# Optimization experiments

Hardware: AMD Instinct MI355X
Metric: run time of the kernel (lower is better)

## Reference

```python
import jax, jax.numpy as jnp
import numpy as np

N_NODES = 100000
N_EDGES = 300000
N_BOUNDARY = 1024
N_VERTS = 4        # n_verts[i]; selects out_layers[3] = Linear(fc_n, 12)
CONVS = [3, 64, 128, 256]
FC_N = 256


def _uniform(k, shape, fan_in):
    s = 1.0 / np.sqrt(fan_in)
    return jax.random.uniform(k, shape, minval=-s, maxval=s, dtype=jnp.float32)


def setup_inputs() -> dict:
    key = jax.random.key(0)
    ks = jax.random.split(key, 32)
    inp = {}
    inp['vs'] = jax.random.normal(ks[0], (N_NODES, 3), dtype=jnp.float32)
    inp['edges'] = jax.random.randint(ks[1], (N_EDGES, 2), 0, N_NODES)
    inp['boundary_idx'] = jax.random.randint(ks[2], (N_BOUNDARY,), 0, N_NODES)
    inp['n_verts'] = N_VERTS
    ki = 3
    for j in range(len(CONVS) - 1):
        cin, cout = CONVS[j], CONVS[j + 1]
        inp[f'W_self{j}'] = _uniform(ks[ki], (cin, cout), cin); ki += 1
        inp[f'W_nbr{j}'] = _uniform(ks[ki], (cin, cout), cin); ki += 1
        inp[f'b{j}'] = _uniform(ks[ki], (cout,), cin); ki += 1
    inp['W_dense'] = _uniform(ks[ki], (CONVS[-1], FC_N), CONVS[-1]); ki += 1
    inp['b_dense'] = _uniform(ks[ki], (FC_N,), CONVS[-1]); ki += 1
    inp['W_out'] = _uniform(ks[ki], (FC_N, 3 * N_VERTS), FC_N); ki += 1
    inp['b_out'] = _uniform(ks[ki], (3 * N_VERTS,), FC_N)
    return inp


def graph_conv(x, edges, W_self, W_nbr, b):
    # out_i = x_i @ W_self + (sum_{j in N(i)} x_j) @ W_nbr + b, symmetric edges
    n = x.shape[0]
    src, dst = edges[:, 0], edges[:, 1]
    agg = jax.ops.segment_sum(x[src], dst, num_segments=n)
    agg = agg + jax.ops.segment_sum(x[dst], src, num_segments=n)
    return x @ W_self + agg @ W_nbr + b


def reference(vs, edges, boundary_idx, n_verts,
              W_self0, W_nbr0, b0, W_self1, W_nbr1, b1, W_self2, W_nbr2, b2,
              W_dense, b_dense, W_out, b_out):
    boundary_mean = jnp.mean(vs[boundary_idx], axis=0)  # (3,)
    x = vs
    for Ws, Wn, b in ((W_self0, W_nbr0, b0), (W_self1, W_nbr1, b1), (W_self2, W_nbr2, b2)):
        x = jax.nn.relu(graph_conv(x, edges, Ws, Wn, b))
    pooled = jnp.mean(x[boundary_idx], axis=0, keepdims=True)  # (1, C)
    h = jax.nn.relu(pooled @ W_dense + b_dense)                # (1, FC_N)
    out = (h @ W_out + b_out).reshape((n_verts, 3))
    return boundary_mean + out
```

## Files before the change

kernel.cpp:

```cpp
#include <hip/hip_runtime.h>

#define N_NODES 100000
#define N_EDGES 300000
#define NB 1024

#define CAP_F1 16384
#define CAP_F2 65536
#define K_ADJ  64

#define CNT_F1 0
#define CNT_F2 16

#define OFF_X1C     0u
#define OFF_X2C     4194304u
#define OFF_X3B     6291456u
#define OFF_AGG0C   6553600u
#define OFF_AGG1C   6815744u
#define OFF_AGG2C   7864320u
#define OFF_POOL    7995392u
#define OFF_CNT     7995648u
#define OFF_DEGF2   7995712u
#define OFF_DEGF1   8061248u
#define OFF_DEGB    8077632u
#define OFF_MF1     8078656u
#define OFF_MF2     8178656u
#define ZERO_END    8278656u
#define ZERO_BYTES  ((ZERO_END - OFF_POOL) * 4u)
#define OFF_SLOTB   8278656u
#define FF_BYTES    (100000u * 4u)
#define OFF_SLOTF1  8378656u
#define OFF_SLOTF2  8478656u
#define OFF_LISTF1  8578656u
#define OFF_LISTF2  8595040u
#define OFF_ADJ0    8660576u
#define OFF_ADJF1   12854880u
#define OFF_ADJB    13903456u
#define OFF_IDXX2   13968992u
#define OFF_IDXA2   13970016u
#define OFF_F1F2    13971040u
#define OFF_BMEAN   13987424u

__global__ void bmean_kernel(const float* __restrict__ vs, const int* __restrict__ bidx,
                             float* __restrict__ bmean) {
    int tid = threadIdx.x;
    float s0 = 0.f, s1 = 0.f, s2 = 0.f;
    for (int i = tid; i < NB; i += 256) {
        int n = bidx[i];
        s0 += vs[n * 3 + 0];
        s1 += vs[n * 3 + 1];
        s2 += vs[n * 3 + 2];
    }
    for (int off = 32; off > 0; off >>= 1) {
        s0 += __shfl_down(s0, off);
        s1 += __shfl_down(s1, off);
        s2 += __shfl_down(s2, off);
    }
    __shared__ float red[4][3];
    int wave = tid >> 6;
    if ((tid & 63) == 0) { red[wave][0] = s0; red[wave][1] = s1; red[wave][2] = s2; }
    __syncthreads();
    if (tid == 0) {
        float t0 = 0, t1 = 0, t2 = 0;
        for (int w = 0; w < 4; w++) { t0 += red[w][0]; t1 += red[w][1]; t2 += red[w][2]; }
        bmean[0] = t0 / NB; bmean[1] = t1 / NB; bmean[2] = t2 / NB;
    }
}

__global__ void mark_b_kernel(const int* __restrict__ bidx, int* __restrict__ slotB) {
    int i = blockIdx.x * 256 + threadIdx.x;
    if (i < NB) slotB[bidx[i]] = i;
}

__global__ void scan_mark_kernel(const int2* __restrict__ edges, const int* __restrict__ srcSlot,
                                 int* __restrict__ mark) {
    int e = blockIdx.x * 256 + threadIdx.x;
    if (e >= N_EDGES) return;
    int2 ed = edges[e];
    if (srcSlot[ed.y] >= 0) mark[ed.x] = 1;
    if (srcSlot[ed.x] >= 0) mark[ed.y] = 1;
}

__global__ __launch_bounds__(256) void compact_kernel(
        const int* __restrict__ mark, const int* __restrict__ aux,
        int* __restrict__ slot, int* __restrict__ list,
        int* __restrict__ cnt, int cap, int* __restrict__ f1map) {
    int i = blockIdx.x * 256 + threadIdx.x;
    int auxv = -1;
    bool want = false;
    if (i < N_NODES) {
        auxv = aux[i];
        want = (mark[i] != 0) || (auxv >= 0);
    }
    int wave = threadIdx.x >> 6, lane = threadIdx.x & 63;
    unsigned long long m = __ballot(want);
    int rank = __popcll(m & ((1ull << lane) - 1));
    __shared__ int s_w[4];
    __shared__ int s_base;
    if (lane == 0) s_w[wave] = __popcll(m);
    __syncthreads();
    if (threadIdx.x == 0) {
        int s = 0;
        #pragma unroll
        for (int w = 0; w < 4; w++) { int v = s_w[w]; s_w[w] = s; s += v; }
        s_base = s ? atomicAdd(cnt, s) : 0;
    }
    __syncthreads();
    if (i < N_NODES) {
        int p = -1;
        if (want) {
            p = s_base + s_w[wave] + rank;
            if (p < cap) list[p] = i; else p = -1;
        }
        slot[i] = p;
        if (f1map && auxv >= 0) f1map[auxv] = p;
    }
}

__device__ __forceinline__ void adj_append(int* __restrict__ deg, int* __restrict__ adj,
                                           int slot, int src) {
    int pos = atomicAdd(&deg[slot], 1);
    if (pos < K_ADJ) adj[slot * K_ADJ + pos] = src;
}

__global__ void build_adj_kernel(const int2* __restrict__ edges,
                                 const int* __restrict__ slotB, const int* __restrict__ slotF1,
                                 const int* __restrict__ slotF2,
                                 int* __restrict__ degF2, int* __restrict__ adj0,
                                 int* __restrict__ degF1, int* __restrict__ adjF1,
                                 int* __restrict__ degB, int* __restrict__ adjB) {
    int e = blockIdx.x * 256 + threadIdx.x;
    if (e >= N_EDGES) return;
    int2 ed = edges[e];
    int x = ed.x, y = ed.y;
    int sxB = slotB[x], syB = slotB[y];
    int sxF1 = slotF1[x], syF1 = slotF1[y];
    int sxF2 = slotF2[x], syF2 = slotF2[y];
    if (syF2 >= 0) adj_append(degF2, adj0, syF2, x);
    if (sxF2 >= 0) adj_append(degF2, adj0, sxF2, y);
    if (syF1 >= 0) adj_append(degF1, adjF1, syF1, sxF2);
    if (sxF1 >= 0) adj_append(degF1, adjF1, sxF1, syF2);
    if (syB >= 0)  adj_append(degB, adjB, syB, sxF1);
    if (sxB >= 0)  adj_append(degB, adjB, sxB, syF1);
}

__global__ void conv2_idx_kernel(const int* __restrict__ bidx, const int* __restrict__ slotB,
                                 const int* __restrict__ slotF1,
                                 int* __restrict__ idxx, int* __restrict__ idxa) {
    int i = blockIdx.x * 256 + threadIdx.x;
    if (i >= NB) return;
    int n = bidx[i];
    idxx[i] = slotF1[n];
    idxa[i] = slotB[n];
}

__global__ void gather0_kernel(const float* __restrict__ vs, const int* __restrict__ adj0,
                               const int* __restrict__ degF2, const int* __restrict__ cnt,
                               float* __restrict__ agg0c) {
    int s = blockIdx.x * 256 + threadIdx.x;
    int n = min(cnt[CNT_F2], CAP_F2);
    if (s >= n) return;
    int deg = min(degF2[s], K_ADJ);
    float a0 = 0.f, a1 = 0.f, a2 = 0.f;
    for (int d = 0; d < deg; d++) {
        int src = adj0[s * K_ADJ + d];
        a0 += vs[src * 3 + 0];
        a1 += vs[src * 3 + 1];
        a2 += vs[src * 3 + 2];
    }
    agg0c[s * 4 + 0] = a0; agg0c[s * 4 + 1] = a1; agg0c[s * 4 + 2] = a2;
}

__global__ void conv0c_kernel(const float* __restrict__ vs, const int* __restrict__ listF2,
                              const float* __restrict__ agg0c,
                              const float* __restrict__ Ws, const float* __restrict__ Wn,
                              const float* __restrict__ b, const int* __restrict__ cnt,
                              float* __restrict__ x1c) {
    int nF2 = min(cnt[CNT_F2], CAP_F2);
    if ((int)blockIdx.x * 4 >= nF2) return;
    __shared__ float ws_l[192], wn_l[192], b_l[64];
    int tid = threadIdx.x;
    if (tid < 192) { ws_l[tid] = Ws[tid]; wn_l[tid] = Wn[tid]; }
    if (tid < 64) b_l[tid] = b[tid];
    __syncthreads();
    int g = blockIdx.x * 4 + (tid >> 6);
    int j = tid & 63;
    if (g >= nF2) return;
    int n = listF2[g];
    float x0 = vs[n * 3 + 0], x1v = vs[n * 3 + 1], x2v = vs[n * 3 + 2];
    float a0 = agg0c[g * 4 + 0], a1 = agg0c[g * 4 + 1], a2 = agg0c[g * 4 + 2];
    float acc = b_l[j];
    acc = fmaf(x0, ws_l[0 * 64 + j], acc);
    acc = fmaf(x1v, ws_l[1 * 64 + j], acc);
    acc = fmaf(x2v, ws_l[2 * 64 + j], acc);
    acc = fmaf(a0, wn_l[0 * 64 + j], acc);
    acc = fmaf(a1, wn_l[1 * 64 + j], acc);
    acc = fmaf(a2, wn_l[2 * 64 + j], acc);
    x1c[g * 64 + j] = fmaxf(acc, 0.f);
}

__global__ __launch_bounds__(256) void gather1_kernel(const float* __restrict__ x1c,
                                                      const int* __restrict__ adjF1,
                                                      const int* __restrict__ degF1,
                                                      const int* __restrict__ cnt,
                                                      float* __restrict__ agg1c) {
    int wslot = blockIdx.x * 4 + (threadIdx.x >> 6);
    int lane = threadIdx.x & 63;
    int n = min(cnt[CNT_F1], CAP_F1);
    if (wslot >= n) return;
    int deg = min(degF1[wslot], K_ADJ);
    float acc = 0.f;
    for (int d = 0; d < deg; d++) {
        int src = adjF1[wslot * K_ADJ + d];
        if (src >= 0) acc += x1c[src * 64 + lane];
    }
    agg1c[wslot * 64 + lane] = acc;
}

__global__ __launch_bounds__(256) void gather2_kernel(const float* __restrict__ x2c,
                                                      const int* __restrict__ adjB,
                                                      const int* __restrict__ degB,
                                                      float* __restrict__ agg2c) {
    int wslot = blockIdx.x * 4 + (threadIdx.x >> 6);
    int lane = threadIdx.x & 63;
    int deg = min(degB[wslot], K_ADJ);
    float a0 = 0.f, a1 = 0.f;
    for (int d = 0; d < deg; d++) {
        int src = adjB[wslot * K_ADJ + d];
        if (src >= 0) {
            a0 += x2c[src * 128 + lane];
            a1 += x2c[src * 128 + 64 + lane];
        }
    }
    agg2c[wslot * 128 + lane] = a0;
    agg2c[wslot * 128 + 64 + lane] = a1;
}

template <int CIN, int COUT, int ROWS>
__global__ __launch_bounds__(256) void convT_kernel(
    const float* __restrict__ x, const float* __restrict__ agg,
    const float* __restrict__ Ws, const float* __restrict__ Wn,
    const float* __restrict__ b, float* __restrict__ out,
    const int* __restrict__ idxx, const int* __restrict__ idxa,
    int nrows_max, const int* __restrict__ nrows_dev) {
    const int RPT = ROWS / 4;
    const int C4 = CIN / 4;
    const int UNR = 16;
    __shared__ float xs[ROWS * CIN];
    __shared__ float as[ROWS * CIN];
    int nrows = nrows_max;
    if (nrows_dev) { int nd = nrows_dev[0]; nrows = nd < nrows ? nd : nrows; }
    int gbase = blockIdx.x * ROWS;
    if (gbase >= nrows) return;
    int tid = threadIdx.x;
    int cb = blockIdx.y * 64;
    for (int i = tid; i < ROWS * C4; i += 256) {
        int nl = i / C4, c4 = i % C4;
        int ng = gbase + nl;
        float4 xv = make_float4(0.f, 0.f, 0.f, 0.f);
        float4 av = xv;
        if (ng < nrows) {
            int rowx = idxx ? idxx[ng] : ng;
            int rowa = idxa ? idxa[ng] : ng;
            xv = ((const float4*)x)[rowx * C4 + c4];
            av = ((const float4*)agg)[rowa * C4 + c4];
        }
        ((float4*)xs)[i] = xv;
        ((float4*)as)[i] = av;
    }
    __syncthreads();
    int j = tid & 63, g = tid >> 6;
    const float* Wsp = Ws + cb + j;
    const float* Wnp = Wn + cb + j;
    float acc[RPT];
    float bv = b[cb + j];
    #pragma unroll
    for (int k = 0; k < RPT; k++) acc[k] = bv;
    float w0[2 * UNR];
    #pragma unroll
    for (int u = 0; u < UNR; u++) {
        w0[u]       = Wsp[u * COUT];
        w0[UNR + u] = Wnp[u * COUT];
    }
    for (int cc = 0; cc < CIN; cc += UNR) {
        float w1[2 * UNR];
        bool more = (cc + UNR) < CIN;
        if (more) {
            #pragma unroll
            for (int u = 0; u < UNR; u++) {
                w1[u]       = Wsp[(cc + UNR + u) * COUT];
                w1[UNR + u] = Wnp[(cc + UNR + u) * COUT];
            }
        }
        #pragma unroll
        for (int u = 0; u < UNR; u++) {
            float wsv = w0[u], wnv = w0[UNR + u];
            #pragma unroll
            for (int k = 0; k < RPT; k++) {
                float xv = xs[(g * RPT + k) * CIN + cc + u];
                float av = as[(g * RPT + k) * CIN + cc + u];
                acc[k] = fmaf(xv, wsv, fmaf(av, wnv, acc[k]));
            }
        }
        if (more) {
            #pragma unroll
            for (int u = 0; u < 2 * UNR; u++) w0[u] = w1[u];
        }
    }
    #pragma unroll
    for (int k = 0; k < RPT; k++) {
        int ng = gbase + g * RPT + k;
        if (ng < nrows) out[ng * COUT + cb + j] = fmaxf(acc[k], 0.f);
    }
}

__global__ void pool_kernel(const float* __restrict__ x3b, float* __restrict__ pooled) {
    int j = threadIdx.x;
    int r0 = blockIdx.x * 32;
    float s = 0.f;
    for (int r = 0; r < 32; r++) s += x3b[(r0 + r) * 256 + j];
    atomicAdd(&pooled[j], s);
}

__global__ void head_kernel(const float* __restrict__ pooled_sum, const float* __restrict__ bmean,
                            const float* __restrict__ Wd, const float* __restrict__ bd,
                            const float* __restrict__ Wo, const float* __restrict__ bo,
                            float* __restrict__ out) {
    __shared__ float p_l[256], h_l[256];
    int tid = threadIdx.x;
    p_l[tid] = pooled_sum[tid] * (1.0f / NB);
    __syncthreads();
    float acc = bd[tid];
    for (int c = 0; c < 256; c++) acc = fmaf(p_l[c], Wd[c * 256 + tid], acc);
    h_l[tid] = fmaxf(acc, 0.f);
    __syncthreads();
    if (tid < 12) {
        float o = bo[tid];
        for (int c = 0; c < 256; c++) o = fmaf(h_l[c], Wo[c * 12 + tid], o);
        out[tid] = o + bmean[tid % 3];
    }
}

extern "C" void kernel_launch(void* const* d_in, const int* in_sizes, int n_in,
                              void* d_out, int out_size, void* d_ws, size_t ws_size,
                              hipStream_t stream) {
    const float* vs    = (const float*)d_in[0];
    const int2*  edges = (const int2*)d_in[1];
    const int*   bidx  = (const int*)d_in[2];
    const float* Ws0 = (const float*)d_in[4];
    const float* Wn0 = (const float*)d_in[5];
    const float* b0  = (const float*)d_in[6];
    const float* Ws1 = (const float*)d_in[7];
    const float* Wn1 = (const float*)d_in[8];
    const float* b1  = (const float*)d_in[9];
    const float* Ws2 = (const float*)d_in[10];
    const float* Wn2 = (const float*)d_in[11];
    const float* b2  = (const float*)d_in[12];
    const float* Wd  = (const float*)d_in[13];
    const float* bd  = (const float*)d_in[14];
    const float* Wo  = (const float*)d_in[15];
    const float* bo  = (const float*)d_in[16];

    float* ws = (float*)d_ws;
    float* x1c    = ws + OFF_X1C;
    float* x2c    = ws + OFF_X2C;
    float* x3b    = ws + OFF_X3B;
    float* agg0c  = ws + OFF_AGG0C;
    float* agg1c  = ws + OFF_AGG1C;
    float* agg2c  = ws + OFF_AGG2C;
    float* pooled = ws + OFF_POOL;
    int*   cnt    = (int*)(ws + OFF_CNT);
    int*   degF2  = (int*)(ws + OFF_DEGF2);
    int*   degF1  = (int*)(ws + OFF_DEGF1);
    int*   degB   = (int*)(ws + OFF_DEGB);
    int*   mF1    = (int*)(ws + OFF_MF1);
    int*   mF2    = (int*)(ws + OFF_MF2);
    int*   slotB  = (int*)(ws + OFF_SLOTB);
    int*   slotF1 = (int*)(ws + OFF_SLOTF1);
    int*   slotF2 = (int*)(ws + OFF_SLOTF2);
    int*   listF1 = (int*)(ws + OFF_LISTF1);
    int*   listF2 = (int*)(ws + OFF_LISTF2);
    int*   adj0   = (int*)(ws + OFF_ADJ0);
    int*   adjF1  = (int*)(ws + OFF_ADJF1);
    int*   adjB   = (int*)(ws + OFF_ADJB);
    int*   idxx2  = (int*)(ws + OFF_IDXX2);
    int*   idxa2  = (int*)(ws + OFF_IDXA2);
    int*   f1f2   = (int*)(ws + OFF_F1F2);
    float* bmean  = ws + OFF_BMEAN;
    float* outp   = (float*)d_out;

    const int EB = (N_EDGES + 255) / 256;
    const int NBLK = (N_NODES + 255) / 256;

    hipMemsetAsync(ws + OFF_POOL, 0, ZERO_BYTES, stream);
    hipMemsetAsync(ws + OFF_SLOTB, 0xFF, FF_BYTES, stream);

    bmean_kernel<<<1, 256, 0, stream>>>(vs, bidx, bmean);

    mark_b_kernel<<<(NB + 255) / 256, 256, 0, stream>>>(bidx, slotB);
    scan_mark_kernel<<<EB, 256, 0, stream>>>(edges, slotB, mF1);
    compact_kernel<<<NBLK, 256, 0, stream>>>(mF1, slotB, slotF1, listF1,
                                             cnt + CNT_F1, CAP_F1, nullptr);
    scan_mark_kernel<<<EB, 256, 0, stream>>>(edges, slotF1, mF2);
    compact_kernel<<<NBLK, 256, 0, stream>>>(mF2, slotF1, slotF2, listF2,
                                             cnt + CNT_F2, CAP_F2, f1f2);
    build_adj_kernel<<<EB, 256, 0, stream>>>(edges, slotB, slotF1, slotF2,
                                             degF2, adj0, degF1, adjF1, degB, adjB);
    conv2_idx_kernel<<<(NB + 255) / 256, 256, 0, stream>>>(bidx, slotB, slotF1, idxx2, idxa2);

    gather0_kernel<<<CAP_F2 / 256, 256, 0, stream>>>(vs, adj0, degF2, cnt, agg0c);
    conv0c_kernel<<<CAP_F2 / 4, 256, 0, stream>>>(vs, listF2, agg0c, Ws0, Wn0, b0, cnt, x1c);

    gather1_kernel<<<CAP_F1 / 4, 256, 0, stream>>>(x1c, adjF1, degF1, cnt, agg1c);
    convT_kernel<64, 128, 16><<<dim3(CAP_F1 / 16, 2), 256, 0, stream>>>(
        x1c, agg1c, Ws1, Wn1, b1, x2c, f1f2, nullptr, CAP_F1, cnt + CNT_F1);

    gather2_kernel<<<NB / 4, 256, 0, stream>>>(x2c, adjB, degB, agg2c);
    convT_kernel<128, 256, 8><<<dim3(NB / 8, 4), 256, 0, stream>>>(
        x2c, agg2c, Ws2, Wn2, b2, x3b, idxx2, idxa2, NB, nullptr);

    pool_kernel<<<32, 256, 0, stream>>>(x3b, pooled);
    head_kernel<<<1, 256, 0, stream>>>(pooled, bmean, Wd, bd, Wo, bo, outp);
}
```

Baseline: 232.9 us.

## Fuse frontier-building stages into one cooperative kernel and fuse gather/pool into convs

Replaces the chain of small preprocessing kernels (boundary mean, marking, two compactions, adjacency build, index setup) with a single cooperative kernel that separates phases with grid-wide syncs. The layer-0 neighbor gather is folded into the conv0 kernel using one wave per node and a shuffle reduction, and pooling is folded into the last conv through shared and global atomics. This cuts launch overhead and intermediate buffers, but grid.sync costs and the fixed 1024-block cooperative grid may limit parallelism. The pooled sum's floating-point order now depends on atomic timing.

```diff
diff --git a/kernel.cpp b/kernel.cpp
--- a/kernel.cpp
+++ b/kernel.cpp
@@ -1,4 +1,7 @@
 #include <hip/hip_runtime.h>
+#include <hip/hip_cooperative_groups.h>
+
+namespace cg = cooperative_groups;
 
 #define N_NODES 100000
 #define N_EDGES 300000
@@ -11,10 +14,11 @@
 #define CNT_F1 0
 #define CNT_F2 16
 
+#define FGRID  1024
+
 #define OFF_X1C     0u
 #define OFF_X2C     4194304u
 #define OFF_X3B     6291456u
-#define OFF_AGG0C   6553600u
 #define OFF_AGG1C   6815744u
 #define OFF_AGG2C   7864320u
 #define OFF_POOL    7995392u
@@ -38,143 +42,143 @@
 #define OFF_IDXX2   13968992u
 #define OFF_IDXA2   13970016u
 #define OFF_F1F2    13971040u
-#define OFF_BMEAN   13987424u
-
-__global__ void bmean_kernel(const float* __restrict__ vs, const int* __restrict__ bidx,
-                             float* __restrict__ bmean) {
-    int tid = threadIdx.x;
-    float s0 = 0.f, s1 = 0.f, s2 = 0.f;
-    for (int i = tid; i < NB; i += 256) {
-        int n = bidx[i];
-        s0 += vs[n * 3 + 0];
-        s1 += vs[n * 3 + 1];
-        s2 += vs[n * 3 + 2];
-    }
-    for (int off = 32; off > 0; off >>= 1) {
-        s0 += __shfl_down(s0, off);
-        s1 += __shfl_down(s1, off);
-        s2 += __shfl_down(s2, off);
-    }
-    __shared__ float red[4][3];
-    int wave = tid >> 6;
-    if ((tid & 63) == 0) { red[wave][0] = s0; red[wave][1] = s1; red[wave][2] = s2; }
-    __syncthreads();
-    if (tid == 0) {
-        float t0 = 0, t1 = 0, t2 = 0;
-        for (int w = 0; w < 4; w++) { t0 += red[w][0]; t1 += red[w][1]; t2 += red[w][2]; }
-        bmean[0] = t0 / NB; bmean[1] = t1 / NB; bmean[2] = t2 / NB;
-    }
-}
-
-__global__ void mark_b_kernel(const int* __restrict__ bidx, int* __restrict__ slotB) {
-    int i = blockIdx.x * 256 + threadIdx.x;
-    if (i < NB) slotB[bidx[i]] = i;
-}
-
-__global__ void scan_mark_kernel(const int2* __restrict__ edges, const int* __restrict__ srcSlot,
-                                 int* __restrict__ mark) {
-    int e = blockIdx.x * 256 + threadIdx.x;
-    if (e >= N_EDGES) return;
-    int2 ed = edges[e];
-    if (srcSlot[ed.y] >= 0) mark[ed.x] = 1;
-    if (srcSlot[ed.x] >= 0) mark[ed.y] = 1;
-}
-
-__global__ __launch_bounds__(256) void compact_kernel(
+#define OFF_BSUM    13987424u
+#define OFF_BMEAN   13990496u
+
+struct FArgs {
+    const float* vs; const int2* edges; const int* bidx;
+    int* slotB; int* mF1; int* slotF1; int* listF1;
+    int* mF2; int* slotF2; int* listF2; int* f1f2;
+    int* cnt; int* degF2; int* adj0; int* degF1; int* adjF1;
+    int* degB; int* adjB; int* idxx; int* idxa;
+    float* bsum; float* bmean;
+};
+
+__device__ __forceinline__ void adj_append(int* __restrict__ deg, int* __restrict__ adj,
+                                           int slot, int src) {
+    int pos = atomicAdd(&deg[slot], 1);
+    if (pos < K_ADJ) adj[slot * K_ADJ + pos] = src;
+}
+
+__device__ __forceinline__ void compact_phase(
+        int i, int lane, int wave, int tidx,
         const int* __restrict__ mark, const int* __restrict__ aux,
         int* __restrict__ slot, int* __restrict__ list,
-        int* __restrict__ cnt, int cap, int* __restrict__ f1map) {
-    int i = blockIdx.x * 256 + threadIdx.x;
+        int* __restrict__ cnt, int cap, int* __restrict__ f1map,
+        int* s_w, int* s_base) {
     int auxv = -1;
     bool want = false;
     if (i < N_NODES) {
         auxv = aux[i];
         want = (mark[i] != 0) || (auxv >= 0);
     }
-    int wave = threadIdx.x >> 6, lane = threadIdx.x & 63;
     unsigned long long m = __ballot(want);
     int rank = __popcll(m & ((1ull << lane) - 1));
-    __shared__ int s_w[4];
-    __shared__ int s_base;
     if (lane == 0) s_w[wave] = __popcll(m);
     __syncthreads();
-    if (threadIdx.x == 0) {
+    if (tidx == 0) {
         int s = 0;
         #pragma unroll
         for (int w = 0; w < 4; w++) { int v = s_w[w]; s_w[w] = s; s += v; }
-        s_base = s ? atomicAdd(cnt, s) : 0;
+        s_base[0] = s ? atomicAdd(cnt, s) : 0;
     }
     __syncthreads();
     if (i < N_NODES) {
         int p = -1;
         if (want) {
-            p = s_base + s_w[wave] + rank;
+            p = s_base[0] + s_w[wave] + rank;
             if (p < cap) list[p] = i; else p = -1;
         }
         slot[i] = p;
         if (f1map && auxv >= 0) f1map[auxv] = p;
     }
-}
-
-__device__ __forceinline__ void adj_append(int* __restrict__ deg, int* __restrict__ adj,
-                                           int slot, int src) {
-    int pos = atomicAdd(&deg[slot], 1);
-    if (pos < K_ADJ) adj[slot * K_ADJ + pos] = src;
-}
-
-__global__ void build_adj_kernel(const int2* __restrict__ edges,
-                                 const int* __restrict__ slotB, const int* __restrict__ slotF1,
-                                 const int* __restrict__ slotF2,
-                                 int* __restrict__ degF2, int* __restrict__ adj0,
-                                 int* __restrict__ degF1, int* __restrict__ adjF1,
-                                 int* __restrict__ degB, int* __restrict__ adjB) {
-    int e = blockIdx.x * 256 + threadIdx.x;
-    if (e >= N_EDGES) return;
-    int2 ed = edges[e];
-    int x = ed.x, y = ed.y;
-    int sxB = slotB[x], syB = slotB[y];
-    int sxF1 = slotF1[x], syF1 = slotF1[y];
-    int sxF2 = slotF2[x], syF2 = slotF2[y];
-    if (syF2 >= 0) adj_append(degF2, adj0, syF2, x);
-    if (sxF2 >= 0) adj_append(degF2, adj0, sxF2, y);
-    if (syF1 >= 0) adj_append(degF1, adjF1, syF1, sxF2);
-    if (sxF1 >= 0) adj_append(degF1, adjF1, sxF1, syF2);
-    if (syB >= 0)  adj_append(degB, adjB, syB, sxF1);
-    if (sxB >= 0)  adj_append(degB, adjB, sxB, syF1);
-}
-
-__global__ void conv2_idx_kernel(const int* __restrict__ bidx, const int* __restrict__ slotB,
-                                 const int* __restrict__ slotF1,
-                                 int* __restrict__ idxx, int* __restrict__ idxa) {
-    int i = blockIdx.x * 256 + threadIdx.x;
-    if (i >= NB) return;
-    int n = bidx[i];
-    idxx[i] = slotF1[n];
-    idxa[i] = slotB[n];
-}
-
-__global__ void gather0_kernel(const float* __restrict__ vs, const int* __restrict__ adj0,
-                               const int* __restrict__ degF2, const int* __restrict__ cnt,
-                               float* __restrict__ agg0c) {
-    int s = blockIdx.x * 256 + threadIdx.x;
-    int n = min(cnt[CNT_F2], CAP_F2);
-    if (s >= n) return;
-    int deg = min(degF2[s], K_ADJ);
-    float a0 = 0.f, a1 = 0.f, a2 = 0.f;
-    for (int d = 0; d < deg; d++) {
-        int src = adj0[s * K_ADJ + d];
-        a0 += vs[src * 3 + 0];
-        a1 += vs[src * 3 + 1];
-        a2 += vs[src * 3 + 2];
-    }
-    agg0c[s * 4 + 0] = a0; agg0c[s * 4 + 1] = a1; agg0c[s * 4 + 2] = a2;
-}
-
-__global__ void conv0c_kernel(const float* __restrict__ vs, const int* __restrict__ listF2,
-                              const float* __restrict__ agg0c,
-                              const float* __restrict__ Ws, const float* __restrict__ Wn,
-                              const float* __restrict__ b, const int* __restrict__ cnt,
-                              float* __restrict__ x1c) {
+    __syncthreads();
+}
+
+__global__ void __launch_bounds__(256) frontier_kernel(FArgs a) {
+    cg::grid_group grid = cg::this_grid();
+    const int tid0 = blockIdx.x * 256 + threadIdx.x;
+    const int stride = gridDim.x * 256;
+    const int lane = threadIdx.x & 63, wave = threadIdx.x >> 6;
+    __shared__ int s_w[4];
+    __shared__ int s_base[1];
+    __shared__ float s_red[4][3];
+
+    float s0 = 0.f, s1 = 0.f, s2 = 0.f;
+    for (int i = tid0; i < NB; i += stride) {
+        int n = a.bidx[i];
+        a.slotB[n] = i;
+        s0 += a.vs[n * 3 + 0]; s1 += a.vs[n * 3 + 1]; s2 += a.vs[n * 3 + 2];
+    }
+    for (int off = 32; off > 0; off >>= 1) {
+        s0 += __shfl_down(s0, off); s1 += __shfl_down(s1, off); s2 += __shfl_down(s2, off);
+    }
+    if (lane == 0) { s_red[wave][0] = s0; s_red[wave][1] = s1; s_red[wave][2] = s2; }
+    __syncthreads();
+    if (threadIdx.x == 0) {
+        float t0 = 0, t1 = 0, t2 = 0;
+        for (int w = 0; w < 4; w++) { t0 += s_red[w][0]; t1 += s_red[w][1]; t2 += s_red[w][2]; }
+        a.bsum[blockIdx.x * 3 + 0] = t0;
+        a.bsum[blockIdx.x * 3 + 1] = t1;
+        a.bsum[blockIdx.x * 3 + 2] = t2;
+    }
+    grid.sync();
+
+    for (int e = tid0; e < N_EDGES; e += stride) {
+        int2 ed = a.edges[e];
+        if (a.slotB[ed.y] >= 0) a.mF1[ed.x] = 1;
+        if (a.slotB[ed.x] >= 0) a.mF1[ed.y] = 1;
+    }
+    if (blockIdx.x == 0 && threadIdx.x < 192) {
+        int c = threadIdx.x >> 6, l = threadIdx.x & 63;
+        float p = 0.f;
+        for (int k = l; k < (int)gridDim.x; k += 64) p += a.bsum[k * 3 + c];
+        for (int off = 32; off > 0; off >>= 1) p += __shfl_down(p, off);
+        if (l == 0) a.bmean[c] = p / NB;
+    }
+    grid.sync();
+
+    compact_phase(tid0, lane, wave, threadIdx.x, a.mF1, a.slotB,
+                  a.slotF1, a.listF1, a.cnt + CNT_F1, CAP_F1, nullptr, s_w, s_base);
+    grid.sync();
+
+    for (int e = tid0; e < N_EDGES; e += stride) {
+        int2 ed = a.edges[e];
+        if (a.slotF1[ed.y] >= 0) a.mF2[ed.x] = 1;
+        if (a.slotF1[ed.x] >= 0) a.mF2[ed.y] = 1;
+    }
+    grid.sync();
+
+    compact_phase(tid0, lane, wave, threadIdx.x, a.mF2, a.slotF1,
+                  a.slotF2, a.listF2, a.cnt + CNT_F2, CAP_F2, a.f1f2, s_w, s_base);
+    grid.sync();
+
+    for (int e = tid0; e < N_EDGES; e += stride) {
+        int2 ed = a.edges[e];
+        int x = ed.x, y = ed.y;
+        int sxB = a.slotB[x], syB = a.slotB[y];
+        int sxF1 = a.slotF1[x], syF1 = a.slotF1[y];
+        int sxF2 = a.slotF2[x], syF2 = a.slotF2[y];
+        if (syF2 >= 0) adj_append(a.degF2, a.adj0, syF2, x);
+        if (sxF2 >= 0) adj_append(a.degF2, a.adj0, sxF2, y);
+        if (syF1 >= 0) adj_append(a.degF1, a.adjF1, syF1, sxF2);
+        if (sxF1 >= 0) adj_append(a.degF1, a.adjF1, sxF1, syF2);
+        if (syB >= 0)  adj_append(a.degB, a.adjB, syB, sxF1);
+        if (sxB >= 0)  adj_append(a.degB, a.adjB, sxB, syF1);
+    }
+    for (int i = tid0; i < NB; i += stride) {
+        int n = a.bidx[i];
+        a.idxx[i] = a.slotF1[n];
+        a.idxa[i] = a.slotB[n];
+    }
+}
+
+__global__ __launch_bounds__(256) void conv0f_kernel(
+        const float* __restrict__ vs, const int* __restrict__ listF2,
+        const int* __restrict__ adj0, const int* __restrict__ degF2,
+        const float* __restrict__ Ws, const float* __restrict__ Wn,
+        const float* __restrict__ b, const int* __restrict__ cnt,
+        float* __restrict__ x1c) {
     int nF2 = min(cnt[CNT_F2], CAP_F2);
     if ((int)blockIdx.x * 4 >= nF2) return;
     __shared__ float ws_l[192], wn_l[192], b_l[64];
@@ -182,20 +186,29 @@
     if (tid < 192) { ws_l[tid] = Ws[tid]; wn_l[tid] = Wn[tid]; }
     if (tid < 64) b_l[tid] = b[tid];
     __syncthreads();
-    int g = blockIdx.x * 4 + (tid >> 6);
-    int j = tid & 63;
-    if (g >= nF2) return;
-    int n = listF2[g];
+    int s = blockIdx.x * 4 + (tid >> 6);
+    int lane = tid & 63;
+    if (s >= nF2) return;
+    int deg = min(degF2[s], K_ADJ);
+    float a0 = 0.f, a1 = 0.f, a2 = 0.f;
+    if (lane < deg) {
+        int src = adj0[s * K_ADJ + lane];
+        a0 = vs[src * 3 + 0]; a1 = vs[src * 3 + 1]; a2 = vs[src * 3 + 2];
+    }
+    for (int off = 32; off > 0; off >>= 1) {
+        a0 += __shfl_down(a0, off); a1 += __shfl_down(a1, off); a2 += __shfl_down(a2, off);
+    }
+    a0 = __shfl(a0, 0); a1 = __shfl(a1, 0); a2 = __shfl(a2, 0);
+    int n = listF2[s];
     float x0 = vs[n * 3 + 0], x1v = vs[n * 3 + 1], x2v = vs[n * 3 + 2];
-    float a0 = agg0c[g * 4 + 0], a1 = agg0c[g * 4 + 1], a2 = agg0c[g * 4 + 2];
-    float acc = b_l[j];
-    acc = fmaf(x0, ws_l[0 * 64 + j], acc);
-    acc = fmaf(x1v, ws_l[1 * 64 + j], acc);
-    acc = fmaf(x2v, ws_l[2 * 64 + j], acc);
-    acc = fmaf(a0, wn_l[0 * 64 + j], acc);
-    acc = fmaf(a1, wn_l[1 * 64 + j], acc);
-    acc = fmaf(a2, wn_l[2 * 64 + j], acc);
-    x1c[g * 64 + j] = fmaxf(acc, 0.f);
+    float acc = b_l[lane];
+    acc = fmaf(x0, ws_l[0 * 64 + lane], acc);
+    acc = fmaf(x1v, ws_l[1 * 64 + lane], acc);
+    acc = fmaf(x2v, ws_l[2 * 64 + lane], acc);
+    acc = fmaf(a0, wn_l[0 * 64 + lane], acc);
+    acc = fmaf(a1, wn_l[1 * 64 + lane], acc);
+    acc = fmaf(a2, wn_l[2 * 64 + lane], acc);
+    x1c[s * 64 + lane] = fmaxf(acc, 0.f);
 }
 
 __global__ __launch_bounds__(256) void gather1_kernel(const float* __restrict__ x1c,
@@ -235,7 +248,7 @@
     agg2c[wslot * 128 + 64 + lane] = a1;
 }
 
-template <int CIN, int COUT, int ROWS>
+template <int CIN, int COUT, int ROWS, bool POOL>
 __global__ __launch_bounds__(256) void convT_kernel(
     const float* __restrict__ x, const float* __restrict__ agg,
     const float* __restrict__ Ws, const float* __restrict__ Wn,
@@ -247,12 +260,14 @@
     const int UNR = 16;
     __shared__ float xs[ROWS * CIN];
     __shared__ float as[ROWS * CIN];
+    __shared__ float psum[64];
     int nrows = nrows_max;
     if (nrows_dev) { int nd = nrows_dev[0]; nrows = nd < nrows ? nd : nrows; }
     int gbase = blockIdx.x * ROWS;
     if (gbase >= nrows) return;
     int tid = threadIdx.x;
     int cb = blockIdx.y * 64;
+    if (POOL && tid < 64) psum[tid] = 0.f;
     for (int i = tid; i < ROWS * C4; i += 256) {
         int nl = i / C4, c4 = i % C4;
         int ng = gbase + nl;
@@ -306,19 +321,23 @@
             for (int u = 0; u < 2 * UNR; u++) w0[u] = w1[u];
         }
     }
-    #pragma unroll
-    for (int k = 0; k < RPT; k++) {
-        int ng = gbase + g * RPT + k;
-        if (ng < nrows) out[ng * COUT + cb + j] = fmaxf(acc[k], 0.f);
-    }
-}
-
-__global__ void pool_kernel(const float* __restrict__ x3b, float* __restrict__ pooled) {
-    int j = threadIdx.x;
-    int r0 = blockIdx.x * 32;
-    float s = 0.f;
-    for (int r = 0; r < 32; r++) s += x3b[(r0 + r) * 256 + j];
-    atomicAdd(&pooled[j], s);
+    if (POOL) {
+        float part = 0.f;
+        #pragma unroll
+        for (int k = 0; k < RPT; k++) {
+            int ng = gbase + g * RPT + k;
+            if (ng < nrows) part += fmaxf(acc[k], 0.f);
+        }
+        atomicAdd(&psum[j], part);
+        __syncthreads();
+        if (tid < 64) atomicAdd(&out[cb + tid], psum[tid]);
+    } else {
+        #pragma unroll
+        for (int k = 0; k < RPT; k++) {
+            int ng = gbase + g * RPT + k;
+            if (ng < nrows) out[ng * COUT + cb + j] = fmaxf(acc[k], 0.f);
+        }
+    }
 }
 
 __global__ void head_kernel(const float* __restrict__ pooled_sum, const float* __restrict__ bmean,
@@ -363,61 +382,52 @@
     float* ws = (float*)d_ws;
     float* x1c    = ws + OFF_X1C;
     float* x2c    = ws + OFF_X2C;
-    float* x3b    = ws + OFF_X3B;
-    float* agg0c  = ws + OFF_AGG0C;
     float* agg1c  = ws + OFF_AGG1C;
     float* agg2c  = ws + OFF_AGG2C;
     float* pooled = ws + OFF_POOL;
     int*   cnt    = (int*)(ws + OFF_CNT);
-    int*   degF2  = (int*)(ws + OFF_DEGF2);
-    int*   degF1  = (int*)(ws + OFF_DEGF1);
-    int*   degB   = (int*)(ws + OFF_DEGB);
-    int*   mF1    = (int*)(ws + OFF_MF1);
-    int*   mF2    = (int*)(ws + OFF_MF2);
-    int*   slotB  = (int*)(ws + OFF_SLOTB);
-    int*   slotF1 = (int*)(ws + OFF_SLOTF1);
-    int*   slotF2 = (int*)(ws + OFF_SLOTF2);
-    int*   listF1 = (int*)(ws + OFF_LISTF1);
-    int*   listF2 = (int*)(ws + OFF_LISTF2);
-    int*   adj0   = (int*)(ws + OFF_ADJ0);
-    int*   adjF1  = (int*)(ws + OFF_ADJF1);
-    int*   adjB   = (int*)(ws + OFF_ADJB);
-    int*   idxx2  = (int*)(ws + OFF_IDXX2);
-    int*   idxa2  = (int*)(ws + OFF_IDXA2);
-    int*   f1f2   = (int*)(ws + OFF_F1F2);
     float* bmean  = ws + OFF_BMEAN;
     float* outp   = (float*)d_out;
 
-    const int EB = (N_EDGES + 255) / 256;
-    const int NBLK = (N_NODES + 255) / 256;
+    FArgs fa;
+    fa.vs = vs; fa.edges = edges; fa.bidx = bidx;
+    fa.slotB  = (int*)(ws + OFF_SLOTB);
+    fa.mF1    = (int*)(ws + OFF_MF1);
+    fa.slotF1 = (int*)(ws + OFF_SLOTF1);
+    fa.listF1 = (int*)(ws + OFF_LISTF1);
+    fa.mF2    = (int*)(ws + OFF_MF2);
+    fa.slotF2 = (int*)(ws + OFF_SLOTF2);
+    fa.listF2 = (int*)(ws + OFF_LISTF2);
+    fa.f1f2   = (int*)(ws + OFF_F1F2);
+    fa.cnt    = cnt;
+    fa.degF2  = (int*)(ws + OFF_DEGF2);
+    fa.adj0   = (int*)(ws + OFF_ADJ0);
+    fa.degF1  = (int*)(ws + OFF_DEGF1);
+    fa.adjF1  = (int*)(ws + OFF_ADJF1);
+    fa.degB   = (int*)(ws + OFF_DEGB);
+    fa.adjB   = (int*)(ws + OFF_ADJB);
+    fa.idxx   = (int*)(ws + OFF_IDXX2);
+    fa.idxa   = (int*)(ws + OFF_IDXA2);
+    fa.bsum   = ws + OFF_BSUM;
+    fa.bmean  = bmean;
 
     hipMemsetAsync(ws + OFF_POOL, 0, ZERO_BYTES, stream);
     hipMemsetAsync(ws + OFF_SLOTB, 0xFF, FF_BYTES, stream);
 
-    bmean_kernel<<<1, 256, 0, stream>>>(vs, bidx, bmean);
-
-    mark_b_kernel<<<(NB + 255) / 256, 256, 0, stream>>>(bidx, slotB);
-    scan_mark_kernel<<<EB, 256, 0, stream>>>(edges, slotB, mF1);
-    compact_kernel<<<NBLK, 256, 0, stream>>>(mF1, slotB, slotF1, listF1,
-                                             cnt + CNT_F1, CAP_F1, nullptr);
-    scan_mark_kernel<<<EB, 256, 0, stream>>>(edges, slotF1, mF2);
-    compact_kernel<<<NBLK, 256, 0, stream>>>(mF2, slotF1, slotF2, listF2,
-                                             cnt + CNT_F2, CAP_F2, f1f2);
-    build_adj_kernel<<<EB, 256, 0, stream>>>(edges, slotB, slotF1, slotF2,
-                                             degF2, adj0, degF1, adjF1, degB, adjB);
-    conv2_idx_kernel<<<(NB + 255) / 256, 256, 0, stream>>>(bidx, slotB, slotF1, idxx2, idxa2);
-
-    gather0_kernel<<<CAP_F2 / 256, 256, 0, stream>>>(vs, adj0, degF2, cnt, agg0c);
-    conv0c_kernel<<<CAP_F2 / 4, 256, 0, stream>>>(vs, listF2, agg0c, Ws0, Wn0, b0, cnt, x1c);
-
-    gather1_kernel<<<CAP_F1 / 4, 256, 0, stream>>>(x1c, adjF1, degF1, cnt, agg1c);
-    convT_kernel<64, 128, 16><<<dim3(CAP_F1 / 16, 2), 256, 0, stream>>>(
-        x1c, agg1c, Ws1, Wn1, b1, x2c, f1f2, nullptr, CAP_F1, cnt + CNT_F1);
-
-    gather2_kernel<<<NB / 4, 256, 0, stream>>>(x2c, adjB, degB, agg2c);
-    convT_kernel<128, 256, 8><<<dim3(NB / 8, 4), 256, 0, stream>>>(
-        x2c, agg2c, Ws2, Wn2, b2, x3b, idxx2, idxa2, NB, nullptr);
-
-    pool_kernel<<<32, 256, 0, stream>>>(x3b, pooled);
+    void* kargs[] = { (void*)&fa };
+    hipLaunchCooperativeKernel((const void*)frontier_kernel,
+                               dim3(FGRID), dim3(256), kargs, 0, stream);
+
+    conv0f_kernel<<<CAP_F2 / 4, 256, 0, stream>>>(
+        vs, fa.listF2, fa.adj0, fa.degF2, Ws0, Wn0, b0, cnt, x1c);
+
+    gather1_kernel<<<CAP_F1 / 4, 256, 0, stream>>>(x1c, fa.adjF1, fa.degF1, cnt, agg1c);
+    convT_kernel<64, 128, 16, false><<<dim3(CAP_F1 / 16, 2), 256, 0, stream>>>(
+        x1c, agg1c, Ws1, Wn1, b1, x2c, fa.f1f2, nullptr, CAP_F1, cnt + CNT_F1);
+
+    gather2_kernel<<<NB / 4, 256, 0, stream>>>(x2c, fa.adjB, fa.degB, agg2c);
+    convT_kernel<128, 256, 8, true><<<dim3(NB / 8, 4), 256, 0, stream>>>(
+        x2c, agg2c, Ws2, Wn2, b2, pooled, fa.idxx, fa.idxa, NB, nullptr);
+
     head_kernel<<<1, 256, 0, stream>>>(pooled, bmean, Wd, bd, Wo, bo, outp);
 }
```

New measurement: 808.2 us. 247% more time.

## Fuse layer-0 gather into conv and pooling into final conv epilogue

Applied to the files above, without the earlier changes.

Merges the layer-0 neighbour gather into the conv0 kernel, using one wavefront per node with lane-parallel neighbour loads and a shuffle reduction. Folds the mean-pool into the last graph-conv kernel via shared-memory atomics followed by global atomics. This drops two kernel launches and the agg0/x3 intermediate buffers. In exchange it adds atomic contention on the pooled vector and summation order that varies between runs.

```diff
diff --git a/kernel.cpp b/kernel.cpp
--- a/kernel.cpp
+++ b/kernel.cpp
@@ -13,8 +13,6 @@
 
 #define OFF_X1C     0u
 #define OFF_X2C     4194304u
-#define OFF_X3B     6291456u
-#define OFF_AGG0C   6553600u
 #define OFF_AGG1C   6815744u
 #define OFF_AGG2C   7864320u
 #define OFF_POOL    7995392u
@@ -153,28 +151,12 @@
     idxa[i] = slotB[n];
 }
 
-__global__ void gather0_kernel(const float* __restrict__ vs, const int* __restrict__ adj0,
-                               const int* __restrict__ degF2, const int* __restrict__ cnt,
-                               float* __restrict__ agg0c) {
-    int s = blockIdx.x * 256 + threadIdx.x;
-    int n = min(cnt[CNT_F2], CAP_F2);
-    if (s >= n) return;
-    int deg = min(degF2[s], K_ADJ);
-    float a0 = 0.f, a1 = 0.f, a2 = 0.f;
-    for (int d = 0; d < deg; d++) {
-        int src = adj0[s * K_ADJ + d];
-        a0 += vs[src * 3 + 0];
-        a1 += vs[src * 3 + 1];
-        a2 += vs[src * 3 + 2];
-    }
-    agg0c[s * 4 + 0] = a0; agg0c[s * 4 + 1] = a1; agg0c[s * 4 + 2] = a2;
-}
-
-__global__ void conv0c_kernel(const float* __restrict__ vs, const int* __restrict__ listF2,
-                              const float* __restrict__ agg0c,
-                              const float* __restrict__ Ws, const float* __restrict__ Wn,
-                              const float* __restrict__ b, const int* __restrict__ cnt,
-                              float* __restrict__ x1c) {
+__global__ __launch_bounds__(256) void conv0f_kernel(
+        const float* __restrict__ vs, const int* __restrict__ listF2,
+        const int* __restrict__ adj0, const int* __restrict__ degF2,
+        const float* __restrict__ Ws, const float* __restrict__ Wn,
+        const float* __restrict__ b, const int* __restrict__ cnt,
+        float* __restrict__ x1c) {
     int nF2 = min(cnt[CNT_F2], CAP_F2);
     if ((int)blockIdx.x * 4 >= nF2) return;
     __shared__ float ws_l[192], wn_l[192], b_l[64];
@@ -182,20 +164,29 @@
     if (tid < 192) { ws_l[tid] = Ws[tid]; wn_l[tid] = Wn[tid]; }
     if (tid < 64) b_l[tid] = b[tid];
     __syncthreads();
-    int g = blockIdx.x * 4 + (tid >> 6);
-    int j = tid & 63;
-    if (g >= nF2) return;
-    int n = listF2[g];
+    int s = blockIdx.x * 4 + (tid >> 6);
+    int lane = tid & 63;
+    if (s >= nF2) return;
+    int deg = min(degF2[s], K_ADJ);
+    float a0 = 0.f, a1 = 0.f, a2 = 0.f;
+    if (lane < deg) {
+        int src = adj0[s * K_ADJ + lane];
+        a0 = vs[src * 3 + 0]; a1 = vs[src * 3 + 1]; a2 = vs[src * 3 + 2];
+    }
+    for (int off = 32; off > 0; off >>= 1) {
+        a0 += __shfl_down(a0, off); a1 += __shfl_down(a1, off); a2 += __shfl_down(a2, off);
+    }
+    a0 = __shfl(a0, 0); a1 = __shfl(a1, 0); a2 = __shfl(a2, 0);
+    int n = listF2[s];
     float x0 = vs[n * 3 + 0], x1v = vs[n * 3 + 1], x2v = vs[n * 3 + 2];
-    float a0 = agg0c[g * 4 + 0], a1 = agg0c[g * 4 + 1], a2 = agg0c[g * 4 + 2];
-    float acc = b_l[j];
-    acc = fmaf(x0, ws_l[0 * 64 + j], acc);
-    acc = fmaf(x1v, ws_l[1 * 64 + j], acc);
-    acc = fmaf(x2v, ws_l[2 * 64 + j], acc);
-    acc = fmaf(a0, wn_l[0 * 64 + j], acc);
-    acc = fmaf(a1, wn_l[1 * 64 + j], acc);
-    acc = fmaf(a2, wn_l[2 * 64 + j], acc);
-    x1c[g * 64 + j] = fmaxf(acc, 0.f);
+    float acc = b_l[lane];
+    acc = fmaf(x0, ws_l[0 * 64 + lane], acc);
+    acc = fmaf(x1v, ws_l[1 * 64 + lane], acc);
+    acc = fmaf(x2v, ws_l[2 * 64 + lane], acc);
+    acc = fmaf(a0, wn_l[0 * 64 + lane], acc);
+    acc = fmaf(a1, wn_l[1 * 64 + lane], acc);
+    acc = fmaf(a2, wn_l[2 * 64 + lane], acc);
+    x1c[s * 64 + lane] = fmaxf(acc, 0.f);
 }
 
 __global__ __launch_bounds__(256) void gather1_kernel(const float* __restrict__ x1c,
@@ -235,7 +226,7 @@
     agg2c[wslot * 128 + 64 + lane] = a1;
 }
 
-template <int CIN, int COUT, int ROWS>
+template <int CIN, int COUT, int ROWS, bool POOL>
 __global__ __launch_bounds__(256) void convT_kernel(
     const float* __restrict__ x, const float* __restrict__ agg,
     const float* __restrict__ Ws, const float* __restrict__ Wn,
@@ -247,12 +238,14 @@
     const int UNR = 16;
     __shared__ float xs[ROWS * CIN];
     __shared__ float as[ROWS * CIN];
+    __shared__ float psum[64];
     int nrows = nrows_max;
     if (nrows_dev) { int nd = nrows_dev[0]; nrows = nd < nrows ? nd : nrows; }
     int gbase = blockIdx.x * ROWS;
     if (gbase >= nrows) return;
     int tid = threadIdx.x;
     int cb = blockIdx.y * 64;
+    if (POOL && tid < 64) psum[tid] = 0.f;
     for (int i = tid; i < ROWS * C4; i += 256) {
         int nl = i / C4, c4 = i % C4;
         int ng = gbase + nl;
@@ -306,19 +299,23 @@
             for (int u = 0; u < 2 * UNR; u++) w0[u] = w1[u];
         }
     }
-    #pragma unroll
-    for (int k = 0; k < RPT; k++) {
-        int ng = gbase + g * RPT + k;
-        if (ng < nrows) out[ng * COUT + cb + j] = fmaxf(acc[k], 0.f);
-    }
-}
-
-__global__ void pool_kernel(const float* __restrict__ x3b, float* __restrict__ pooled) {
-    int j = threadIdx.x;
-    int r0 = blockIdx.x * 32;
-    float s = 0.f;
-    for (int r = 0; r < 32; r++) s += x3b[(r0 + r) * 256 + j];
-    atomicAdd(&pooled[j], s);
+    if (POOL) {
+        float part = 0.f;
+        #pragma unroll
+        for (int k = 0; k < RPT; k++) {
+            int ng = gbase + g * RPT + k;
+            if (ng < nrows) part += fmaxf(acc[k], 0.f);
+        }
+        atomicAdd(&psum[j], part);
+        __syncthreads();
+        if (tid < 64) atomicAdd(&out[cb + tid], psum[tid]);
+    } else {
+        #pragma unroll
+        for (int k = 0; k < RPT; k++) {
+            int ng = gbase + g * RPT + k;
+            if (ng < nrows) out[ng * COUT + cb + j] = fmaxf(acc[k], 0.f);
+        }
+    }
 }
 
 __global__ void head_kernel(const float* __restrict__ pooled_sum, const float* __restrict__ bmean,
@@ -363,8 +360,6 @@
     float* ws = (float*)d_ws;
     float* x1c    = ws + OFF_X1C;
     float* x2c    = ws + OFF_X2C;
-    float* x3b    = ws + OFF_X3B;
-    float* agg0c  = ws + OFF_AGG0C;
     float* agg1c  = ws + OFF_AGG1C;
     float* agg2c  = ws + OFF_AGG2C;
     float* pooled = ws + OFF_POOL;
@@ -407,17 +402,16 @@
                                              degF2, adj0, degF1, adjF1, degB, adjB);
     conv2_idx_kernel<<<(NB + 255) / 256, 256, 0, stream>>>(bidx, slotB, slotF1, idxx2, idxa2);
 
-    gather0_kernel<<<CAP_F2 / 256, 256, 0, stream>>>(vs, adj0, degF2, cnt, agg0c);
-    conv0c_kernel<<<CAP_F2 / 4, 256, 0, stream>>>(vs, listF2, agg0c, Ws0, Wn0, b0, cnt, x1c);
+    conv0f_kernel<<<CAP_F2 / 4, 256, 0, stream>>>(
+        vs, listF2, adj0, degF2, Ws0, Wn0, b0, cnt, x1c);
 
     gather1_kernel<<<CAP_F1 / 4, 256, 0, stream>>>(x1c, adjF1, degF1, cnt, agg1c);
-    convT_kernel<64, 128, 16><<<dim3(CAP_F1 / 16, 2), 256, 0, stream>>>(
+    convT_kernel<64, 128, 16, false><<<dim3(CAP_F1 / 16, 2), 256, 0, stream>>>(
         x1c, agg1c, Ws1, Wn1, b1, x2c, f1f2, nullptr, CAP_F1, cnt + CNT_F1);
 
     gather2_kernel<<<NB / 4, 256, 0, stream>>>(x2c, adjB, degB, agg2c);
-    convT_kernel<128, 256, 8><<<dim3(NB / 8, 4), 256, 0, stream>>>(
-        x2c, agg2c, Ws2, Wn2, b2, x3b, idxx2, idxa2, NB, nullptr);
-
-    pool_kernel<<<32, 256, 0, stream>>>(x3b, pooled);
+    convT_kernel<128, 256, 8, true><<<dim3(NB / 8, 4), 256, 0, stream>>>(
+        x2c, agg2c, Ws2, Wn2, b2, pooled, idxx2, idxa2, NB, nullptr);
+
     head_kernel<<<1, 256, 0, stream>>>(pooled, bmean, Wd, bd, Wo, bo, outp);
 }
```

After: 231.4 us. About the same (-0.7%).
